# Kernel tuning notes

Measured on AMD Instinct MI355X. Metric: run time of the kernel, lower is better.

The kernel has to match this reference:

```python
import jax, jax.numpy as jnp
import numpy as np

B, S, D, H = 2, 2048, 1024, 16
DEPTH = D // H


def setup_inputs() -> dict:
    key = jax.random.key(0)
    ks = jax.random.split(key, 10)
    batch = jax.random.normal(ks[0], (B, S, D), dtype=jnp.float32)
    # variable-length valid rows, like padded batches in the original repo
    lengths = jax.random.randint(ks[1], (B,), S // 2, S + 1)
    mask = jnp.arange(S)[None, :] < lengths[:, None]  # (B, S) bool
    scale = 1.0 / np.sqrt(D)
    Wq = jax.random.normal(ks[2], (D, D), dtype=jnp.float32) * scale
    bq = jnp.zeros((D,), dtype=jnp.float32)
    Wk = jax.random.normal(ks[3], (D, D), dtype=jnp.float32) * scale
    bk = jnp.zeros((D,), dtype=jnp.float32)
    Wv = jax.random.normal(ks[4], (D, D), dtype=jnp.float32) * scale
    bv = jnp.zeros((D,), dtype=jnp.float32)
    Wo = jax.random.normal(ks[5], (D, D), dtype=jnp.float32) * scale
    bo = jnp.zeros((D,), dtype=jnp.float32)
    return {"batch": batch, "mask": mask, "Wq": Wq, "bq": bq, "Wk": Wk,
            "bk": bk, "Wv": Wv, "bv": bv, "Wo": Wo, "bo": bo}


def _split_heads(x):
    # (B, S, D) -> (B, H, S, depth)
    b, s, _ = x.shape
    return x.reshape(b, s, H, DEPTH).transpose(0, 2, 1, 3)


def reference(batch, mask, Wq, bq, Wk, bk, Wv, bv, Wo, bo):
    b, s, _ = batch.shape
    Q = _split_heads(batch @ Wq + bq)
    K = _split_heads(batch @ Wk + bk)
    V = _split_heads(batch @ Wv + bv)
    # scaled dot-product attention with key-padding mask
    logits = jnp.einsum('bhqd,bhkd->bhqk', Q, K) / jnp.sqrt(
        jnp.asarray(DEPTH, dtype=batch.dtype))
    neg = (~mask).astype(batch.dtype) * -1e9  # (B, S)
    logits = logits + neg[:, None, None, :]
    attn = jax.nn.softmax(logits, axis=-1)
    X = jnp.einsum('bhqk,bhkd->bhqd', attn, V)
    X = X.transpose(0, 2, 1, 3).reshape(b, s, D)
    return X @ Wo + bo
```

## Files before the change

kernel.cpp:

```cpp
#include <hip/hip_runtime.h>
#include <hip/hip_bf16.h>

#define DEV __device__ __forceinline__

typedef short bf16x8 __attribute__((ext_vector_type(8)));
typedef float f32x4  __attribute__((ext_vector_type(4)));
typedef float f32x16 __attribute__((ext_vector_type(16)));

#define Bc 2
#define Sc 2048
#define Dc 1024
#define Hc 16

#define OFF_XB    0u
#define OFF_WQKVT 8388608u
#define OFF_WOT   14680064u
#define OFF_Q     16777216u
#define OFF_K     25165824u
#define OFF_VT    33554432u
#define OFF_XA    41943040u
#define OFF_BIASC 50331648u
#define OFF_LENS  50343936u

DEV short f2bf(float f) {
    __hip_bfloat16 h = __float2bfloat16(f);
    union { __hip_bfloat16 h; short s; } u; u.h = h; return u.s;
}

DEV int cvtpk(float lo, float hi_) {
    int r;
    asm("v_cvt_pk_bf16_f32 %0, %1, %2" : "=v"(r) : "v"(lo), "v"(hi_));
    return r;
}

DEV float vexp2(float x) {
    float r;
    asm("v_exp_f32 %0, %1" : "=v"(r) : "v"(x));
    return r;
}

DEV void gload16(const void* g, void* l) {
    __builtin_amdgcn_global_load_lds((const __attribute__((address_space(1))) void*)g,
                                     (__attribute__((address_space(3))) void*)l, 16, 0, 0);
}

union I4BF { int i[4]; bf16x8 v; };

DEV bf16x8 vread(const char* Vc, int row, int grp, int hi16, int rsw) {
    return *(const bf16x8*)(Vc + row * 128 + ((grp + hi16) ^ rsw));
}

__global__ __launch_bounds__(256) void prep_all_kernel(
    const float* __restrict__ batch,
    const float* __restrict__ Wq, const float* __restrict__ Wk,
    const float* __restrict__ Wv, const float* __restrict__ Wo,
    const float* __restrict__ bq, const float* __restrict__ bk, const float* __restrict__ bv,
    const unsigned char* __restrict__ mask,
    short* __restrict__ XB, short* __restrict__ WQKVT, short* __restrict__ WOT,
    float* __restrict__ biasc, int* __restrict__ lens)
{
    __shared__ float tsm[32][33];
    __shared__ int cnt;
    int blk = blockIdx.x, t = threadIdx.x;

    if (blk < 4096) {
        int i = blk * 256 + t;
        float4 v = ((const float4*)batch)[i];
        short4 o;
        o.x = f2bf(v.x); o.y = f2bf(v.y); o.z = f2bf(v.z); o.w = f2bf(v.w);
        ((short4*)XB)[i] = o;
        return;
    }
    if (blk < 8192) {
        int w = blk - 4096, z = w >> 10, tile = w & 1023;
        const float* src; short* dst;
        if (z == 0)      { src = Wq; dst = WQKVT; }
        else if (z == 1) { src = Wk; dst = WQKVT + 1024 * 1024; }
        else if (z == 2) { src = Wv; dst = WQKVT + 2 * 1024 * 1024; }
        else             { src = Wo; dst = WOT; }
        int tx = t & 31, ty = t >> 5;
        int r0 = (tile >> 5) * 32, c0 = (tile & 31) * 32;
#pragma unroll
        for (int i = 0; i < 4; i++)
            tsm[ty + i * 8][tx] = src[(size_t)(r0 + ty + i * 8) * Dc + c0 + tx];
        __syncthreads();
#pragma unroll
        for (int i = 0; i < 4; i++)
            dst[(size_t)(c0 + ty + i * 8) * Dc + r0 + tx] = f2bf(tsm[tx][ty + i * 8]);
        return;
    }
    if (blk == 8192) {
        for (int i = t; i < Dc; i += 256) {
            biasc[i] = bq[i]; biasc[Dc + i] = bk[i]; biasc[2 * Dc + i] = bv[i];
        }
        return;
    }
    {
        int b = blk - 8193;
        bool is_i32 = (mask[1] == 0);
        if (t == 0) cnt = 0;
        __syncthreads();
        int local = 0;
        for (int s = t; s < Sc; s += 256) {
            bool v = is_i32 ? (((const int*)mask)[b * Sc + s] != 0) : (mask[b * Sc + s] != 0);
            local += v ? 1 : 0;
        }
        atomicAdd(&cnt, local);
        __syncthreads();
        if (t == 0) lens[b] = cnt;
    }
}

__global__ __launch_bounds__(256) void vtrans_kernel(const short* __restrict__ V,
                                                     short* __restrict__ VT,
                                                     const int* __restrict__ lens) {
    __shared__ short t[64][65];
    int tid = threadIdx.x;
    int bh = blockIdx.y, s0 = blockIdx.x * 64;
    int b = bh >> 4;
    int kv_end = ((lens[b] + 63) >> 6) << 6;
    if (s0 >= kv_end) return;
    int rr = tid >> 2, c4 = (tid & 3) * 16;
    const short* vrow = V + ((size_t)bh * Sc + s0 + rr) * 64 + c4;
    *(bf16x8*)&t[rr][c4]     = *(const bf16x8*)(vrow);
    *(bf16x8*)&t[rr][c4 + 8] = *(const bf16x8*)(vrow + 8);
    __syncthreads();
    bf16x8 a, b2;
#pragma unroll
    for (int i = 0; i < 4; i++) {
        a[i]      = t[c4 + i][rr];
        a[4 + i]  = t[c4 + 8 + i][rr];
        b2[i]     = t[c4 + 4 + i][rr];
        b2[4 + i] = t[c4 + 12 + i][rr];
    }
    short* orow = VT + ((size_t)bh * 64 + rr) * Sc + s0 + c4;
    *(bf16x8*)(orow)     = a;
    *(bf16x8*)(orow + 8) = b2;
}

__global__ __launch_bounds__(256) void gemm_qkv_kernel(
    const short* __restrict__ A, const short* __restrict__ BT, const float* __restrict__ bias,
    short* __restrict__ Qp, short* __restrict__ Kp, short* __restrict__ Vp,
    const int* __restrict__ lens)
{
    __shared__ short As[128 * 32];
    __shared__ short Bs[128 * 32];
    int tid = threadIdx.x, lane = tid & 63, wave = tid >> 6;
    int l15 = lane & 15, lhi = lane >> 4;
    int bm = blockIdx.x, bn = blockIdx.y;

    if (bn >= 8) {
        int brow = bm >> 4;
        int s_lo = (bm & 15) * 128;
        int kv_end = ((lens[brow] + 63) >> 6) << 6;
        if (s_lo >= kv_end) return;
    }

    int wm = wave >> 1, wn = wave & 1;

    const f32x4 fzero = {0.f, 0.f, 0.f, 0.f};
    f32x4 acc[4][4];
#pragma unroll
    for (int i = 0; i < 4; i++)
#pragma unroll
        for (int j = 0; j < 4; j++) acc[i][j] = fzero;

    const char* Ab = (const char*)A;
    const char* Bb = (const char*)BT;

    for (int k0 = 0; k0 < 1024; k0 += 32) {
#pragma unroll
        for (int i = 0; i < 2; i++) {
            int o = wave * 2048 + i * 1024 + lane * 16;
            int row = o >> 6, cb = o & 63;
            gload16(Ab + ((size_t)(bm * 128 + row) * 1024 + k0) * 2 + cb,
                    (char*)As + wave * 2048 + i * 1024);
            gload16(Bb + ((size_t)(bn * 128 + row) * 1024 + k0) * 2 + cb,
                    (char*)Bs + wave * 2048 + i * 1024);
        }
        __syncthreads();
        bf16x8 af[4], bfv[4];
#pragma unroll
        for (int i = 0; i < 4; i++) {
            af[i]  = *(const bf16x8*)(As + (wm * 64 + i * 16 + l15) * 32 + lhi * 8);
            bfv[i] = *(const bf16x8*)(Bs + (wn * 64 + i * 16 + l15) * 32 + lhi * 8);
        }
#pragma unroll
        for (int i = 0; i < 4; i++)
#pragma unroll
            for (int j = 0; j < 4; j++)
                acc[i][j] = __builtin_amdgcn_mfma_f32_16x16x32_bf16(af[i], bfv[j], acc[i][j], 0, 0, 0);
        __syncthreads();
    }

#pragma unroll
    for (int i = 0; i < 4; i++)
#pragma unroll
        for (int j = 0; j < 4; j++) {
            int c = bn * 128 + wn * 64 + j * 16 + l15;
            float bc = bias[c];
            int rb = bm * 128 + wm * 64 + i * 16 + 4 * lhi;
#pragma unroll
            for (int reg = 0; reg < 4; reg++) {
                int r = rb + reg;
                float v = acc[i][j][reg] + bc;
                int which = c >> 10, cc = c & 1023, h = cc >> 6, d = cc & 63;
                int b = r >> 11, s = r & 2047;
                int bh = b * Hc + h;
                if (which == 0) v *= 0.18033688f;
                short sv = f2bf(v);
                size_t idx = ((size_t)bh * Sc + s) * 64 + d;
                if (which == 0)      Qp[idx] = sv;
                else if (which == 1) Kp[idx] = sv;
                else                 Vp[idx] = sv;
            }
        }
}

__global__ __launch_bounds__(256) void gemm_out_kernel(
    const short* __restrict__ A, const short* __restrict__ BT, const float* __restrict__ bias,
    float* __restrict__ outF)
{
    __shared__ short As[128 * 32];
    __shared__ short Bs[64 * 32];
    int tid = threadIdx.x, lane = tid & 63, wave = tid >> 6;
    int l15 = lane & 15, lhi = lane >> 4;
    int bm = blockIdx.x, bn = blockIdx.y;

    const f32x4 fzero = {0.f, 0.f, 0.f, 0.f};
    f32x4 acc[2][4];
#pragma unroll
    for (int i = 0; i < 2; i++)
#pragma unroll
        for (int j = 0; j < 4; j++) acc[i][j] = fzero;

    const char* Ab = (const char*)A;
    const char* Bb = (const char*)BT;

    for (int k0 = 0; k0 < 1024; k0 += 32) {
#pragma unroll
        for (int i = 0; i < 2; i++) {
            int o = wave * 2048 + i * 1024 + lane * 16;
            int row = o >> 6, cb = o & 63;
            gload16(Ab + ((size_t)(bm * 128 + row) * 1024 + k0) * 2 + cb,
                    (char*)As + wave * 2048 + i * 1024);
        }
        {
            int o = wave * 1024 + lane * 16;
            int row = o >> 6, cb = o & 63;
            gload16(Bb + ((size_t)(bn * 64 + row) * 1024 + k0) * 2 + cb,
                    (char*)Bs + wave * 1024);
        }
        __syncthreads();
        bf16x8 af[2], bfv[4];
#pragma unroll
        for (int i = 0; i < 2; i++)
            af[i] = *(const bf16x8*)(As + (wave * 32 + i * 16 + l15) * 32 + lhi * 8);
#pragma unroll
        for (int j = 0; j < 4; j++)
            bfv[j] = *(const bf16x8*)(Bs + (j * 16 + l15) * 32 + lhi * 8);
#pragma unroll
        for (int i = 0; i < 2; i++)
#pragma unroll
            for (int j = 0; j < 4; j++)
                acc[i][j] = __builtin_amdgcn_mfma_f32_16x16x32_bf16(af[i], bfv[j], acc[i][j], 0, 0, 0);
        __syncthreads();
    }

#pragma unroll
    for (int i = 0; i < 2; i++)
#pragma unroll
        for (int j = 0; j < 4; j++) {
            int c = bn * 64 + j * 16 + l15;
            float bc = bias[c];
            int rb = bm * 128 + wave * 32 + i * 16 + 4 * lhi;
#pragma unroll
            for (int reg = 0; reg < 4; reg++)
                outF[(size_t)(rb + reg) * Dc + c] = acc[i][j][reg] + bc;
        }
}

__global__ __launch_bounds__(128) void attn_kernel(
    const short* __restrict__ Qp, const short* __restrict__ Kp, const short* __restrict__ VTp,
    const int* __restrict__ lens, short* __restrict__ Xout)
{
    int tid = threadIdx.x, lane = tid & 63, wave = tid >> 6;
    int l31 = lane & 31, hi = lane >> 5;

    int orig = blockIdx.x;
    int xcd = orig & 7, idx = orig >> 3;
    int j = idx & 3, bx = idx >> 2;
    int bh = ((j >> 1) << 4) + xcd * 2 + (j & 1);
    int b = bh >> 4, h = bh & 15;
    int q0 = bx * 64 + wave * 32;

    __shared__ short Kt[2][64 * 64];
    __shared__ short Vt[2][64 * 64];

    const short* Qb  = Qp + (size_t)bh * Sc * 64;
    const char*  Kb  = (const char*)(Kp + (size_t)bh * Sc * 64);
    const char*  VTb = (const char*)(VTp + (size_t)bh * 64 * Sc);

    bf16x8 qf[4];
#pragma unroll
    for (int kk = 0; kk < 4; kk++)
        qf[kk] = *(const bf16x8*)(Qb + (size_t)(q0 + l31) * 64 + kk * 16 + hi * 8);

    f32x16 xacc0, xacc1, FZV;
#pragma unroll
    for (int r = 0; r < 16; r++) { xacc0[r] = 0.f; xacc1[r] = 0.f; FZV[r] = 0.f; }
    float lreg = 0.f;

    int len = lens[b];
    int nt = (len + 63) >> 6;
    int rsw = (l31 & 7) << 4;
    int hi16 = hi * 16;

#define STAGE(bufi, kt_)                                                              \
    {                                                                                 \
        int k0_ = (kt_) * 64;                                                         \
        _Pragma("unroll")                                                             \
        for (int i = 0; i < 4; i++) {                                                 \
            int o = wave * 1024 + i * 2048 + lane * 16;                               \
            int row = o >> 7, cb = o & 127;                                           \
            int scb = cb ^ ((row & 7) << 4);                                          \
            gload16(Kb + (size_t)(k0_ + row) * 128 + scb,                             \
                    (char*)&Kt[bufi][0] + wave * 1024 + i * 2048);                    \
            gload16(VTb + (size_t)row * (Sc * 2) + (size_t)k0_ * 2 + scb,             \
                    (char*)&Vt[bufi][0] + wave * 1024 + i * 2048);                    \
        }                                                                             \
    }

#define DOHALF(Kc, Vc, ROFF, KBASE, KT)                                               \
    {                                                                                 \
        __builtin_amdgcn_s_setprio(1);                                                \
        bf16x8 kf0 = *(const bf16x8*)((Kc) + (ROFF + l31) * 128 + (hi16 ^ rsw));      \
        f32x16 s = __builtin_amdgcn_mfma_f32_32x32x16_bf16(kf0, qf[0], FZV, 0, 0, 0); \
        _Pragma("unroll")                                                             \
        for (int kk = 1; kk < 4; kk++) {                                              \
            bf16x8 kf = *(const bf16x8*)((Kc) + (ROFF + l31) * 128 +                  \
                                         ((kk * 32 + hi16) ^ rsw));                   \
            s = __builtin_amdgcn_mfma_f32_32x32x16_bf16(kf, qf[kk], s, 0, 0, 0);      \
        }                                                                             \
        __builtin_amdgcn_s_setprio(0);                                                \
        if ((KT) == nt - 1) {                                                         \
            int rem = len - (KT) * 64;                                                \
            if (rem < (KBASE) + 32) {                                                 \
                _Pragma("unroll")                                                     \
                for (int r = 0; r < 16; r++) {                                        \
                    int key0 = (KBASE) + 4 * hi + (r & 3) + 8 * (r >> 2);             \
                    if (key0 >= rem) s[r] = -3.0e38f;                                 \
                }                                                                     \
            }                                                                         \
        }                                                                             \
        _Pragma("unroll")                                                             \
        for (int r = 0; r < 16; r++) s[r] = vexp2(s[r]);                              \
        {                 \
            float a0 = s[0] + s[1],   a1 = s[2] + s[3];                               \
            float a2 = s[4] + s[5],   a3 = s[6] + s[7];                               \
            float a4 = s[8] + s[9],   a5 = s[10] + s[11];                             \
            float a6 = s[12] + s[13], a7 = s[14] + s[15];                             \
            float b0 = a0 + a1, b1 = a2 + a3, b2 = a4 + a5, b3 = a6 + a7;             \
            lreg += (b0 + b1) + (b2 + b3);                                            \
        }                                                                             \
        I4BF u, w;                                                                    \
        u.i[0] = cvtpk(s[0], s[1]);   u.i[1] = cvtpk(s[2], s[3]);                     \
        u.i[2] = cvtpk(s[4], s[5]);   u.i[3] = cvtpk(s[6], s[7]);                     \
        w.i[0] = cvtpk(s[8], s[9]);   w.i[1] = cvtpk(s[10], s[11]);                   \
        w.i[2] = cvtpk(s[12], s[13]); w.i[3] = cvtpk(s[14], s[15]);                   \
        __builtin_amdgcn_s_setprio(1);                                                \
        {                                                                             \
            bf16x8 v0 = vread((Vc), l31,      (KBASE) * 2,      hi16, rsw);           \
            bf16x8 v1 = vread((Vc), 32 + l31, (KBASE) * 2,      hi16, rsw);           \
            xacc0 = __builtin_amdgcn_mfma_f32_32x32x16_bf16(v0, u.v, xacc0, 0, 0, 0); \
            xacc1 = __builtin_amdgcn_mfma_f32_32x32x16_bf16(v1, u.v, xacc1, 0, 0, 0); \
            bf16x8 v2 = vread((Vc), l31,      (KBASE) * 2 + 32, hi16, rsw);           \
            bf16x8 v3 = vread((Vc), 32 + l31, (KBASE) * 2 + 32, hi16, rsw);           \
            xacc0 = __builtin_amdgcn_mfma_f32_32x32x16_bf16(v2, w.v, xacc0, 0, 0, 0); \
            xacc1 = __builtin_amdgcn_mfma_f32_32x32x16_bf16(v3, w.v, xacc1, 0, 0, 0); \
        }                                                                             \
        __builtin_amdgcn_s_setprio(0);                                                \
    }

#define DOTILE(BUFI, KT)                                                              \
    {                                                                                 \
        const char* Kc_ = (const char*)&Kt[BUFI][0];                                  \
        const char* Vc_ = (const char*)&Vt[BUFI][0];                                  \
        DOHALF(Kc_, Vc_, 0, 0, KT);                                                   \
        DOHALF(Kc_, Vc_, 32, 32, KT);                                                 \
    }

    STAGE(0, 0);
    __syncthreads();

    int kt = 0;
    while (kt + 2 <= nt) {
        if (kt + 1 < nt) STAGE(1, kt + 1);
        DOTILE(0, kt);
        __syncthreads();
        if (kt + 2 < nt) STAGE(0, kt + 2);
        DOTILE(1, kt + 1);
        __syncthreads();
        kt += 2;
    }
    if (kt < nt) DOTILE(0, kt);

    float lfull = lreg + __shfl_xor(lreg, 32, 64);
    float rl = 1.0f / lfull;
    short* orow = Xout + (size_t)(b * Sc + q0 + l31) * Dc + h * 64;
#pragma unroll
    for (int g = 0; g < 4; g++) {
        short4 o;
        o.x = f2bf(xacc0[4 * g + 0] * rl);
        o.y = f2bf(xacc0[4 * g + 1] * rl);
        o.z = f2bf(xacc0[4 * g + 2] * rl);
        o.w = f2bf(xacc0[4 * g + 3] * rl);
        *(short4*)(orow + 4 * hi + 8 * g) = o;
    }
#pragma unroll
    for (int g = 0; g < 4; g++) {
        short4 o;
        o.x = f2bf(xacc1[4 * g + 0] * rl);
        o.y = f2bf(xacc1[4 * g + 1] * rl);
        o.z = f2bf(xacc1[4 * g + 2] * rl);
        o.w = f2bf(xacc1[4 * g + 3] * rl);
        *(short4*)(orow + 32 + 4 * hi + 8 * g) = o;
    }
}


extern "C" void kernel_launch(void* const* d_in, const int* in_sizes, int n_in,
                              void* d_out, int out_size, void* d_ws, size_t ws_size,
                              hipStream_t stream) {
    const float* batch = (const float*)d_in[0];
    const unsigned char* mask = (const unsigned char*)d_in[1];
    const float* Wq = (const float*)d_in[2];
    const float* bq = (const float*)d_in[3];
    const float* Wk = (const float*)d_in[4];
    const float* bk = (const float*)d_in[5];
    const float* Wv = (const float*)d_in[6];
    const float* bv = (const float*)d_in[7];
    const float* Wo = (const float*)d_in[8];
    const float* bo = (const float*)d_in[9];

    char* ws = (char*)d_ws;
    short* XB    = (short*)(ws + OFF_XB);
    short* WQKVT = (short*)(ws + OFF_WQKVT);
    short* WOT   = (short*)(ws + OFF_WOT);
    short* Qb    = (short*)(ws + OFF_Q);
    short* Kb    = (short*)(ws + OFF_K);
    short* VTb   = (short*)(ws + OFF_VT);
    short* XAb   = (short*)(ws + OFF_XA);
    float* BIASC = (float*)(ws + OFF_BIASC);
    int*   LENS  = (int*)(ws + OFF_LENS);
    short* Vscr  = (short*)d_out;

    prep_all_kernel<<<8195, 256, 0, stream>>>(batch, Wq, Wk, Wv, Wo, bq, bk, bv, mask,
                                              XB, WQKVT, WOT, BIASC, LENS);
    gemm_qkv_kernel<<<dim3(32, 24), 256, 0, stream>>>(XB, WQKVT, BIASC, Qb, Kb, Vscr, LENS);
    vtrans_kernel<<<dim3(32, 32), 256, 0, stream>>>(Vscr, VTb, LENS);
    attn_kernel<<<1024, 128, 0, stream>>>(Qb, Kb, VTb, LENS, XAb);
    gemm_out_kernel<<<dim3(32, 16), 256, 0, stream>>>(XAb, WOT, bo, (float*)d_out);
}
```

Measured before the change: 119.5 us.

## Fuse V transpose into QKV GEMM epilogue via swizzled shared memory

The separate vtrans kernel is removed. The QKV GEMM blocks that produce V now stage their accumulator tile in XOR-swizzled shared memory and write V already transposed (per head, depth-major) straight to the VT buffer. This drops one kernel launch and a full write-then-read round trip of V through global memory. In exchange it adds extra LDS traffic, barriers and a serialized two-pass epilogue in the V blocks.

```diff
diff --git a/kernel.cpp b/kernel.cpp
--- a/kernel.cpp
+++ b/kernel.cpp
@@ -111,40 +111,14 @@
     }
 }
 
-__global__ __launch_bounds__(256) void vtrans_kernel(const short* __restrict__ V,
-                                                     short* __restrict__ VT,
-                                                     const int* __restrict__ lens) {
-    __shared__ short t[64][65];
-    int tid = threadIdx.x;
-    int bh = blockIdx.y, s0 = blockIdx.x * 64;
-    int b = bh >> 4;
-    int kv_end = ((lens[b] + 63) >> 6) << 6;
-    if (s0 >= kv_end) return;
-    int rr = tid >> 2, c4 = (tid & 3) * 16;
-    const short* vrow = V + ((size_t)bh * Sc + s0 + rr) * 64 + c4;
-    *(bf16x8*)&t[rr][c4]     = *(const bf16x8*)(vrow);
-    *(bf16x8*)&t[rr][c4 + 8] = *(const bf16x8*)(vrow + 8);
-    __syncthreads();
-    bf16x8 a, b2;
-#pragma unroll
-    for (int i = 0; i < 4; i++) {
-        a[i]      = t[c4 + i][rr];
-        a[4 + i]  = t[c4 + 8 + i][rr];
-        b2[i]     = t[c4 + 4 + i][rr];
-        b2[4 + i] = t[c4 + 12 + i][rr];
-    }
-    short* orow = VT + ((size_t)bh * 64 + rr) * Sc + s0 + c4;
-    *(bf16x8*)(orow)     = a;
-    *(bf16x8*)(orow + 8) = b2;
-}
-
 __global__ __launch_bounds__(256) void gemm_qkv_kernel(
     const short* __restrict__ A, const short* __restrict__ BT, const float* __restrict__ bias,
-    short* __restrict__ Qp, short* __restrict__ Kp, short* __restrict__ Vp,
+    short* __restrict__ Qp, short* __restrict__ Kp, short* __restrict__ VTp,
     const int* __restrict__ lens)
 {
-    __shared__ short As[128 * 32];
-    __shared__ short Bs[128 * 32];
+    __shared__ short SMEM[8192];
+    short* As = SMEM;
+    short* Bs = SMEM + 4096;
     int tid = threadIdx.x, lane = tid & 63, wave = tid >> 6;
     int l15 = lane & 15, lhi = lane >> 4;
     int bm = blockIdx.x, bn = blockIdx.y;
@@ -193,28 +167,76 @@
         __syncthreads();
     }
 
-#pragma unroll
-    for (int i = 0; i < 4; i++)
-#pragma unroll
-        for (int j = 0; j < 4; j++) {
-            int c = bn * 128 + wn * 64 + j * 16 + l15;
-            float bc = bias[c];
-            int rb = bm * 128 + wm * 64 + i * 16 + 4 * lhi;
-#pragma unroll
-            for (int reg = 0; reg < 4; reg++) {
-                int r = rb + reg;
-                float v = acc[i][j][reg] + bc;
-                int which = c >> 10, cc = c & 1023, h = cc >> 6, d = cc & 63;
-                int b = r >> 11, s = r & 2047;
-                int bh = b * Hc + h;
-                if (which == 0) v *= 0.18033688f;
-                short sv = f2bf(v);
-                size_t idx = ((size_t)bh * Sc + s) * 64 + d;
-                if (which == 0)      Qp[idx] = sv;
-                else if (which == 1) Kp[idx] = sv;
-                else                 Vp[idx] = sv;
+    if (bn < 16) {
+#pragma unroll
+        for (int i = 0; i < 4; i++)
+#pragma unroll
+            for (int j = 0; j < 4; j++) {
+                int c = bn * 128 + wn * 64 + j * 16 + l15;
+                float bc = bias[c];
+                int rb = bm * 128 + wm * 64 + i * 16 + 4 * lhi;
+#pragma unroll
+                for (int reg = 0; reg < 4; reg++) {
+                    int r = rb + reg;
+                    float v = acc[i][j][reg] + bc;
+                    int which = c >> 10, cc = c & 1023, h = cc >> 6, d = cc & 63;
+                    int b = r >> 11, s = r & 2047;
+                    int bh = b * Hc + h;
+                    if (which == 0) v *= 0.18033688f;
+                    short sv = f2bf(v);
+                    size_t idx = ((size_t)bh * Sc + s) * 64 + d;
+                    if (which == 0) Qp[idx] = sv;
+                    else            Kp[idx] = sv;
+                }
             }
-        }
+    } else {
+        int b0 = bm >> 4, s0 = (bm & 15) * 128;
+        char* VB = (char*)SMEM;
+#pragma unroll 1
+        for (int hh = 0; hh < 2; hh++) {
+            __syncthreads();
+            if (wn == hh) {
+#pragma unroll
+                for (int i = 0; i < 4; i++)
+#pragma unroll
+                    for (int j = 0; j < 4; j++) {
+                        int c = bn * 128 + wn * 64 + j * 16 + l15;
+                        float bc = bias[c];
+                        int d = j * 16 + l15;
+                        int sp = wm * 64 + i * 16 + 4 * lhi;
+                        short4 pk;
+                        pk.x = f2bf(acc[i][j][0] + bc);
+                        pk.y = f2bf(acc[i][j][1] + bc);
+                        pk.z = f2bf(acc[i][j][2] + bc);
+                        pk.w = f2bf(acc[i][j][3] + bc);
+                        int off = (d * 256 + sp * 2) ^ ((d & 7) << 4);
+                        *(short4*)(VB + off) = pk;
+                    }
+            }
+            __syncthreads();
+            int rr = tid >> 2, c4 = (tid & 3) * 16;
+            int h = (bn - 16) * 2 + hh;
+#pragma unroll
+            for (int g2 = 0; g2 < 2; g2++) {
+                int g = c4 + g2 * 64;
+                bf16x8 a, b2v;
+#pragma unroll
+                for (int i2 = 0; i2 < 4; i2++) {
+                    int o0 = (rr * 256 + (g + i2) * 2)      ^ ((rr & 7) << 4);
+                    int o1 = (rr * 256 + (g + 8 + i2) * 2)  ^ ((rr & 7) << 4);
+                    int o2 = (rr * 256 + (g + 4 + i2) * 2)  ^ ((rr & 7) << 4);
+                    int o3 = (rr * 256 + (g + 12 + i2) * 2) ^ ((rr & 7) << 4);
+                    a[i2]       = *(short*)(VB + o0);
+                    a[4 + i2]   = *(short*)(VB + o1);
+                    b2v[i2]     = *(short*)(VB + o2);
+                    b2v[4 + i2] = *(short*)(VB + o3);
+                }
+                short* orow = VTp + ((size_t)(b0 * Hc + h) * 64 + rr) * Sc + s0 + g;
+                *(bf16x8*)(orow)     = a;
+                *(bf16x8*)(orow + 8) = b2v;
+            }
+        }
+    }
 }
 
 __global__ __launch_bounds__(256) void gemm_out_kernel(
@@ -453,12 +475,10 @@
     short* XAb   = (short*)(ws + OFF_XA);
     float* BIASC = (float*)(ws + OFF_BIASC);
     int*   LENS  = (int*)(ws + OFF_LENS);
-    short* Vscr  = (short*)d_out;
 
     prep_all_kernel<<<8195, 256, 0, stream>>>(batch, Wq, Wk, Wv, Wo, bq, bk, bv, mask,
                                               XB, WQKVT, WOT, BIASC, LENS);
-    gemm_qkv_kernel<<<dim3(32, 24), 256, 0, stream>>>(XB, WQKVT, BIASC, Qb, Kb, Vscr, LENS);
-    vtrans_kernel<<<dim3(32, 32), 256, 0, stream>>>(Vscr, VTb, LENS);
+    gemm_qkv_kernel<<<dim3(32, 24), 256, 0, stream>>>(XB, WQKVT, BIASC, Qb, Kb, VTb, LENS);
     attn_kernel<<<1024, 128, 0, stream>>>(Qb, Kb, VTb, LENS, XAb);
     gemm_out_kernel<<<dim3(32, 16), 256, 0, stream>>>(XAb, WOT, bo, (float*)d_out);
 }
```

New measurement: 127.9 us. 1.07x slower.

## Switch attention to 16x16x32 MFMA with four 16-row waves per block

Applied to the files above, without the earlier changes.

The attention kernel moves from 32x32x16 MFMA tiles on two 32-query waves to 16x16x32 MFMA tiles on four 16-query waves, keeping 64 queries per block. The V transpose kernel's key column order is permuted to match the new P fragment layout, and the row-sum reduction gains an extra shuffle. The aim is more waves per block for latency hiding and smaller accumulators. In exchange, each wave now re-reads every K/V tile from LDS for only 16 queries, which raises LDS traffic per FLOP.

```diff
diff --git a/kernel.cpp b/kernel.cpp
--- a/kernel.cpp
+++ b/kernel.cpp
@@ -5,7 +5,6 @@
 
 typedef short bf16x8 __attribute__((ext_vector_type(8)));
 typedef float f32x4  __attribute__((ext_vector_type(4)));
-typedef float f32x16 __attribute__((ext_vector_type(16)));
 
 #define Bc 2
 #define Sc 2048
@@ -45,10 +44,6 @@
 }
 
 union I4BF { int i[4]; bf16x8 v; };
-
-DEV bf16x8 vread(const char* Vc, int row, int grp, int hi16, int rsw) {
-    return *(const bf16x8*)(Vc + row * 128 + ((grp + hi16) ^ rsw));
-}
 
 __global__ __launch_bounds__(256) void prep_all_kernel(
     const float* __restrict__ batch,
@@ -125,15 +120,18 @@
     *(bf16x8*)&t[rr][c4]     = *(const bf16x8*)(vrow);
     *(bf16x8*)&t[rr][c4 + 8] = *(const bf16x8*)(vrow + 8);
     __syncthreads();
+    int q2 = tid & 3;
+    int gidx = q2 >> 1, half = q2 & 1;
+    int base = gidx * 32, off = half * 8;
     bf16x8 a, b2;
 #pragma unroll
     for (int i = 0; i < 4; i++) {
-        a[i]      = t[c4 + i][rr];
-        a[4 + i]  = t[c4 + 8 + i][rr];
-        b2[i]     = t[c4 + 4 + i][rr];
-        b2[4 + i] = t[c4 + 12 + i][rr];
-    }
-    short* orow = VT + ((size_t)bh * 64 + rr) * Sc + s0 + c4;
+        a[i]      = t[base + off + i][rr];
+        a[4 + i]  = t[base + 16 + off + i][rr];
+        b2[i]     = t[base + off + 4 + i][rr];
+        b2[4 + i] = t[base + 16 + off + 4 + i][rr];
+    }
+    short* orow = VT + ((size_t)bh * 64 + rr) * Sc + s0 + base + half * 16;
     *(bf16x8*)(orow)     = a;
     *(bf16x8*)(orow + 8) = b2;
 }
@@ -280,19 +278,19 @@
         }
 }
 
-__global__ __launch_bounds__(128) void attn_kernel(
+__global__ __launch_bounds__(256) void attn_kernel(
     const short* __restrict__ Qp, const short* __restrict__ Kp, const short* __restrict__ VTp,
     const int* __restrict__ lens, short* __restrict__ Xout)
 {
     int tid = threadIdx.x, lane = tid & 63, wave = tid >> 6;
-    int l31 = lane & 31, hi = lane >> 5;
+    int l15 = lane & 15, g4 = lane >> 4;
 
     int orig = blockIdx.x;
     int xcd = orig & 7, idx = orig >> 3;
     int j = idx & 3, bx = idx >> 2;
     int bh = ((j >> 1) << 4) + xcd * 2 + (j & 1);
     int b = bh >> 4, h = bh & 15;
-    int q0 = bx * 64 + wave * 32;
+    int q0 = bx * 64 + wave * 16;
 
     __shared__ short Kt[2][64 * 64];
     __shared__ short Vt[2][64 * 64];
@@ -301,93 +299,89 @@
     const char*  Kb  = (const char*)(Kp + (size_t)bh * Sc * 64);
     const char*  VTb = (const char*)(VTp + (size_t)bh * 64 * Sc);
 
-    bf16x8 qf[4];
-#pragma unroll
-    for (int kk = 0; kk < 4; kk++)
-        qf[kk] = *(const bf16x8*)(Qb + (size_t)(q0 + l31) * 64 + kk * 16 + hi * 8);
-
-    f32x16 xacc0, xacc1, FZV;
-#pragma unroll
-    for (int r = 0; r < 16; r++) { xacc0[r] = 0.f; xacc1[r] = 0.f; FZV[r] = 0.f; }
+    bf16x8 qf0 = *(const bf16x8*)(Qb + (size_t)(q0 + l15) * 64 + g4 * 8);
+    bf16x8 qf1 = *(const bf16x8*)(Qb + (size_t)(q0 + l15) * 64 + 32 + g4 * 8);
+
+    const f32x4 FZ = {0.f, 0.f, 0.f, 0.f};
+    f32x4 xacc[4];
+#pragma unroll
+    for (int dt = 0; dt < 4; dt++) xacc[dt] = FZ;
     float lreg = 0.f;
 
     int len = lens[b];
     int nt = (len + 63) >> 6;
-    int rsw = (l31 & 7) << 4;
-    int hi16 = hi * 16;
+    int rsw = (l15 & 7) << 4;
+    int g16 = g4 * 16;
 
 #define STAGE(bufi, kt_)                                                              \
     {                                                                                 \
         int k0_ = (kt_) * 64;                                                         \
         _Pragma("unroll")                                                             \
-        for (int i = 0; i < 4; i++) {                                                 \
-            int o = wave * 1024 + i * 2048 + lane * 16;                               \
+        for (int i = 0; i < 2; i++) {                                                 \
+            int o = i * 4096 + tid * 16;                                              \
             int row = o >> 7, cb = o & 127;                                           \
             int scb = cb ^ ((row & 7) << 4);                                          \
             gload16(Kb + (size_t)(k0_ + row) * 128 + scb,                             \
-                    (char*)&Kt[bufi][0] + wave * 1024 + i * 2048);                    \
+                    (char*)&Kt[bufi][0] + o);                                         \
             gload16(VTb + (size_t)row * (Sc * 2) + (size_t)k0_ * 2 + scb,             \
-                    (char*)&Vt[bufi][0] + wave * 1024 + i * 2048);                    \
+                    (char*)&Vt[bufi][0] + o);                                         \
         }                                                                             \
     }
 
-#define DOHALF(Kc, Vc, ROFF, KBASE, KT)                                               \
+#define DOTILE(BUFI, KT)                                                              \
     {                                                                                 \
+        const char* Kc = (const char*)&Kt[BUFI][0];                                   \
+        const char* Vc = (const char*)&Vt[BUFI][0];                                   \
+        f32x4 s[4];                                                                   \
         __builtin_amdgcn_s_setprio(1);                                                \
-        bf16x8 kf0 = *(const bf16x8*)((Kc) + (ROFF + l31) * 128 + (hi16 ^ rsw));      \
-        f32x16 s = __builtin_amdgcn_mfma_f32_32x32x16_bf16(kf0, qf[0], FZV, 0, 0, 0); \
         _Pragma("unroll")                                                             \
-        for (int kk = 1; kk < 4; kk++) {                                              \
-            bf16x8 kf = *(const bf16x8*)((Kc) + (ROFF + l31) * 128 +                  \
-                                         ((kk * 32 + hi16) ^ rsw));                   \
-            s = __builtin_amdgcn_mfma_f32_32x32x16_bf16(kf, qf[kk], s, 0, 0, 0);      \
+        for (int k16 = 0; k16 < 4; k16++) {                                           \
+            const char* kr = Kc + (k16 * 16 + l15) * 128;                             \
+            bf16x8 kf0 = *(const bf16x8*)(kr + (g16 ^ rsw));                          \
+            bf16x8 kf1 = *(const bf16x8*)(kr + ((64 + g16) ^ rsw));                   \
+            s[k16] = __builtin_amdgcn_mfma_f32_16x16x32_bf16(kf0, qf0, FZ, 0, 0, 0);  \
+            s[k16] = __builtin_amdgcn_mfma_f32_16x16x32_bf16(kf1, qf1, s[k16], 0, 0, 0);\
         }                                                                             \
         __builtin_amdgcn_s_setprio(0);                                                \
         if ((KT) == nt - 1) {                                                         \
             int rem = len - (KT) * 64;                                                \
-            if (rem < (KBASE) + 32) {                                                 \
+            if (rem < 64) {                                                           \
                 _Pragma("unroll")                                                     \
-                for (int r = 0; r < 16; r++) {                                        \
-                    int key0 = (KBASE) + 4 * hi + (r & 3) + 8 * (r >> 2);             \
-                    if (key0 >= rem) s[r] = -3.0e38f;                                 \
-                }                                                                     \
+                for (int k16 = 0; k16 < 4; k16++)                                     \
+                    _Pragma("unroll")                                                 \
+                    for (int r = 0; r < 4; r++) {                                     \
+                        int key0 = k16 * 16 + 4 * g4 + r;                             \
+                        if (key0 >= rem) s[k16][r] = -3.0e38f;                        \
+                    }                                                                 \
             }                                                                         \
         }                                                                             \
         _Pragma("unroll")                                                             \
-        for (int r = 0; r < 16; r++) s[r] = vexp2(s[r]);                              \
-        {                 \
-            float a0 = s[0] + s[1],   a1 = s[2] + s[3];                               \
-            float a2 = s[4] + s[5],   a3 = s[6] + s[7];                               \
-            float a4 = s[8] + s[9],   a5 = s[10] + s[11];                             \
-            float a6 = s[12] + s[13], a7 = s[14] + s[15];                             \
-            float b0 = a0 + a1, b1 = a2 + a3, b2 = a4 + a5, b3 = a6 + a7;             \
-            lreg += (b0 + b1) + (b2 + b3);                                            \
+        for (int k16 = 0; k16 < 4; k16++)                                             \
+            _Pragma("unroll")                                                         \
+            for (int r = 0; r < 4; r++) s[k16][r] = vexp2(s[k16][r]);                 \
+        {                                                  \
+            float a0 = (s[0][0] + s[0][1]) + (s[0][2] + s[0][3]);                     \
+            float a1 = (s[1][0] + s[1][1]) + (s[1][2] + s[1][3]);                     \
+            float a2 = (s[2][0] + s[2][1]) + (s[2][2] + s[2][3]);                     \
+            float a3 = (s[3][0] + s[3][1]) + (s[3][2] + s[3][3]);                     \
+            lreg += (a0 + a1) + (a2 + a3);                                            \
         }                                                                             \
-        I4BF u, w;                                                                    \
-        u.i[0] = cvtpk(s[0], s[1]);   u.i[1] = cvtpk(s[2], s[3]);                     \
-        u.i[2] = cvtpk(s[4], s[5]);   u.i[3] = cvtpk(s[6], s[7]);                     \
-        w.i[0] = cvtpk(s[8], s[9]);   w.i[1] = cvtpk(s[10], s[11]);                   \
-        w.i[2] = cvtpk(s[12], s[13]); w.i[3] = cvtpk(s[14], s[15]);                   \
+           \
+        I4BF p0, p1;                                                                  \
+        p0.i[0] = cvtpk(s[0][0], s[0][1]); p0.i[1] = cvtpk(s[0][2], s[0][3]);         \
+        p0.i[2] = cvtpk(s[1][0], s[1][1]); p0.i[3] = cvtpk(s[1][2], s[1][3]);         \
+        p1.i[0] = cvtpk(s[2][0], s[2][1]); p1.i[1] = cvtpk(s[2][2], s[2][3]);         \
+        p1.i[2] = cvtpk(s[3][0], s[3][1]); p1.i[3] = cvtpk(s[3][2], s[3][3]);         \
         __builtin_amdgcn_s_setprio(1);                                                \
-        {                                                                             \
-            bf16x8 v0 = vread((Vc), l31,      (KBASE) * 2,      hi16, rsw);           \
-            bf16x8 v1 = vread((Vc), 32 + l31, (KBASE) * 2,      hi16, rsw);           \
-            xacc0 = __builtin_amdgcn_mfma_f32_32x32x16_bf16(v0, u.v, xacc0, 0, 0, 0); \
-            xacc1 = __builtin_amdgcn_mfma_f32_32x32x16_bf16(v1, u.v, xacc1, 0, 0, 0); \
-            bf16x8 v2 = vread((Vc), l31,      (KBASE) * 2 + 32, hi16, rsw);           \
-            bf16x8 v3 = vread((Vc), 32 + l31, (KBASE) * 2 + 32, hi16, rsw);           \
-            xacc0 = __builtin_amdgcn_mfma_f32_32x32x16_bf16(v2, w.v, xacc0, 0, 0, 0); \
-            xacc1 = __builtin_amdgcn_mfma_f32_32x32x16_bf16(v3, w.v, xacc1, 0, 0, 0); \
+        _Pragma("unroll")                                                             \
+        for (int dt = 0; dt < 4; dt++) {                                              \
+            const char* vr = Vc + (dt * 16 + l15) * 128;                              \
+            bf16x8 v0 = *(const bf16x8*)(vr + (g16 ^ rsw));                           \
+            bf16x8 v1 = *(const bf16x8*)(vr + ((64 + g16) ^ rsw));                    \
+            xacc[dt] = __builtin_amdgcn_mfma_f32_16x16x32_bf16(v0, p0.v, xacc[dt], 0, 0, 0);\
+            xacc[dt] = __builtin_amdgcn_mfma_f32_16x16x32_bf16(v1, p1.v, xacc[dt], 0, 0, 0);\
         }                                                                             \
         __builtin_amdgcn_s_setprio(0);                                                \
-    }
-
-#define DOTILE(BUFI, KT)                                                              \
-    {                                                                                 \
-        const char* Kc_ = (const char*)&Kt[BUFI][0];                                  \
-        const char* Vc_ = (const char*)&Vt[BUFI][0];                                  \
-        DOHALF(Kc_, Vc_, 0, 0, KT);                                                   \
-        DOHALF(Kc_, Vc_, 32, 32, KT);                                                 \
     }
 
     STAGE(0, 0);
@@ -405,26 +399,18 @@
     }
     if (kt < nt) DOTILE(0, kt);
 
-    float lfull = lreg + __shfl_xor(lreg, 32, 64);
+    float lfull = lreg + __shfl_xor(lreg, 16, 64);
+    lfull += __shfl_xor(lfull, 32, 64);
     float rl = 1.0f / lfull;
-    short* orow = Xout + (size_t)(b * Sc + q0 + l31) * Dc + h * 64;
-#pragma unroll
-    for (int g = 0; g < 4; g++) {
+    short* orow = Xout + (size_t)(b * Sc + q0 + l15) * Dc + h * 64;
+#pragma unroll
+    for (int dt = 0; dt < 4; dt++) {
         short4 o;
-        o.x = f2bf(xacc0[4 * g + 0] * rl);
-        o.y = f2bf(xacc0[4 * g + 1] * rl);
-        o.z = f2bf(xacc0[4 * g + 2] * rl);
-        o.w = f2bf(xacc0[4 * g + 3] * rl);
-        *(short4*)(orow + 4 * hi + 8 * g) = o;
-    }
-#pragma unroll
-    for (int g = 0; g < 4; g++) {
-        short4 o;
-        o.x = f2bf(xacc1[4 * g + 0] * rl);
-        o.y = f2bf(xacc1[4 * g + 1] * rl);
-        o.z = f2bf(xacc1[4 * g + 2] * rl);
-        o.w = f2bf(xacc1[4 * g + 3] * rl);
-        *(short4*)(orow + 32 + 4 * hi + 8 * g) = o;
+        o.x = f2bf(xacc[dt][0] * rl);
+        o.y = f2bf(xacc[dt][1] * rl);
+        o.z = f2bf(xacc[dt][2] * rl);
+        o.w = f2bf(xacc[dt][3] * rl);
+        *(short4*)(orow + dt * 16 + 4 * g4) = o;
     }
 }
 
@@ -459,6 +445,6 @@
                                               XB, WQKVT, WOT, BIASC, LENS);
     gemm_qkv_kernel<<<dim3(32, 24), 256, 0, stream>>>(XB, WQKVT, BIASC, Qb, Kb, Vscr, LENS);
     vtrans_kernel<<<dim3(32, 32), 256, 0, stream>>>(Vscr, VTb, LENS);
-    attn_kernel<<<1024, 128, 0, stream>>>(Qb, Kb, VTb, LENS, XAb);
+    attn_kernel<<<1024, 256, 0, stream>>>(Qb, Kb, VTb, LENS, XAb);
     gemm_out_kernel<<<dim3(32, 16), 256, 0, stream>>>(XAb, WOT, bo, (float*)d_out);
 }
```

Result: no change. 119.3 us (-0.2%).
